# Kernel optimization log

Hardware: AMD Instinct MI355X
Metric: run time of the kernel (lower is better)

Reference implementation:

```python
import jax, jax.numpy as jnp
import numpy as np
import math

D_MODEL = 1024
N_HEADS = 16
HEAD_DIM = D_MODEL // N_HEADS
TEMP = 0.1          # sinkhorn temperature
SINK_ITERS = 10     # update_permutation uses n_iterations=10
EPS = 1e-10


def setup_inputs() -> dict:
    key = jax.random.key(0)
    ks = jax.random.split(key, 16)
    b, n, d = 2, 2048, D_MODEL
    x_data = jax.random.normal(ks[0], (b, n, d), dtype=jnp.float32)
    certainty = jax.random.uniform(ks[1], (b, n), dtype=jnp.float32)
    permutation = jnp.stack([jax.random.permutation(jax.random.fold_in(ks[2], i), n)
                             for i in range(b)]).astype(jnp.int64)
    def lin(k):
        kw, kb = jax.random.split(k)
        W = jax.random.normal(kw, (d, d), dtype=jnp.float32) * 0.02
        bvec = jax.random.normal(kb, (d,), dtype=jnp.float32) * 0.02
        return W, bvec
    Wq, bq = lin(ks[3]); Wk, bk = lin(ks[4]); Wv, bv = lin(ks[5]); Wo, bo = lin(ks[6])
    perm_bias_scale = jnp.ones((1, N_HEADS, 1, 1), dtype=jnp.float32)
    certainty_temp = jnp.ones((1,), dtype=jnp.float32) * 2.0
    return {"x_data": x_data, "certainty": certainty, "permutation": permutation,
            "Wq": Wq, "bq": bq, "Wk": Wk, "bk": bk, "Wv": Wv, "bv": bv,
            "Wo": Wo, "bo": bo, "perm_bias_scale": perm_bias_scale,
            "certainty_temp": certainty_temp}


def reference(x_data, certainty, permutation, Wq, bq, Wk, bk, Wv, bv, Wo, bo,
              perm_bias_scale, certainty_temp):
    b, n, d = x_data.shape
    scale = math.sqrt(HEAD_DIM)

    def proj(W, bias):  # nn.Linear: x @ W.T + b, then split heads -> (b,H,n,hd)
        y = jnp.einsum('bnd,ed->bne', x_data, W) + bias
        return y.reshape(b, n, N_HEADS, HEAD_DIM).transpose(0, 2, 1, 3)

    Q, K, V = proj(Wq, bq), proj(Wk, bk), proj(Wv, bv)

    scores = jnp.einsum('bhnk,bhmk->bhnm', Q, K) / scale  # (b,H,n,n)
    # permutation-distance bias: B[i,j] = -|sigma(i)-sigma(j)| * |scale_h|
    pf = permutation.astype(jnp.float32)
    dist = jnp.abs(pf[:, :, None] - pf[:, None, :])       # (b,n,n)
    scores = scores - dist[:, None, :, :] * jnp.abs(perm_bias_scale)

    attention = jax.nn.softmax(scores, axis=-1)           # dropout is identity (eval)
    out = jnp.einsum('bhnm,bhmd->bhnd', attention, V)
    out = out.transpose(0, 2, 1, 3).reshape(b, n, d)
    output = jnp.einsum('bnd,ed->bne', out, Wo) + bo

    # certainty update from attention entropy
    ent = -(attention * jnp.log(attention + EPS)).sum(-1).mean(1)  # (b,n)
    cert_upd = jax.nn.sigmoid(certainty_temp * (math.log(n) - ent))
    new_certainty = jnp.maximum(certainty, cert_upd)

    # permutation update via Sinkhorn on log mean attention
    avg_attn = attention.mean(axis=1)
    P = jnp.exp(jnp.log(avg_attn + EPS) / TEMP)
    def body(_, P):
        P = P / (P.sum(-1, keepdims=True) + EPS)
        P = P / (P.sum(-2, keepdims=True) + EPS)
        return P
    P = jax.lax.fori_loop(0, SINK_ITERS, body, P)
    idx = jnp.argmax(P, axis=-1)                          # (b,n)
    new_permutation = jnp.take_along_axis(permutation, idx, axis=1)

    return output, new_certainty, new_permutation
```

## Files before the change

### kernel.cpp

```cpp
#include <hip/hip_runtime.h>
#include <cstdint>

#define NTOK 2048
#define DMODEL 1024
#define NHEADS 16
#define HD 64
#define BATCH 2
#define EPSF 1e-10f
#define EPSD 1e-10

typedef __attribute__((ext_vector_type(8))) short bf16x8;
typedef __attribute__((ext_vector_type(8))) _Float16 f16x8;
typedef __attribute__((ext_vector_type(4))) float f32x4;

__device__ __forceinline__ float bf2f(unsigned short u){
  union { unsigned int i; float f; } c; c.i = ((unsigned int)u) << 16; return c.f;
}
__device__ __forceinline__ unsigned short f2bf(float f){
  union { float f; unsigned int u; } c; c.f = f;
  unsigned int u = c.u;
  unsigned int r = (u + 0x7FFFu + ((u >> 16) & 1u)) >> 16;
  return (unsigned short)r;
}
__device__ __forceinline__ unsigned short f2h(float f){
  union { _Float16 h; unsigned short u; } c; c.h = (_Float16)f; return c.u;
}
__device__ __forceinline__ float h2f(unsigned short u){
  union { unsigned short u; _Float16 h; } c; c.u = u; return (float)c.h;
}

__device__ __forceinline__ void async16(const unsigned short* g, unsigned short* lds_base){
  __builtin_amdgcn_global_load_lds((const __attribute__((address_space(1))) unsigned int*)g,
                                   (__attribute__((address_space(3))) unsigned int*)lds_base,
                                   16, 0, 0);
}

template<int BM, int BN>
__device__ __forceinline__ void gemm_bt_core(
    const unsigned short* A, int lda,
    const unsigned short* B, int ldb,
    int K,
    f32x4 (&acc)[BM/32][BN/32],
    unsigned short* ldsA, unsigned short* ldsB)
{
  constexpr int TM = BM/32, TN = BN/32;
  const int tid  = threadIdx.x;
  const int lane = tid & 63;
  const int wave = tid >> 6;
  const int wm = wave >> 1, wn = wave & 1;
  const int fr = lane & 15;
  const int fk = (lane >> 4) << 3;
  const int sr = lane >> 2;
  const int sk = (lane & 3) << 3;

  for (int k0 = 0; k0 < K; k0 += 32){
    #pragma unroll
    for (int c = 0; c < BM/64; c++){
      int ch = c*4 + wave;
      async16(A + (long)(ch*16 + sr)*lda + (k0 + sk), ldsA + ch*512);
    }
    #pragma unroll
    for (int c = 0; c < BN/64; c++){
      int ch = c*4 + wave;
      async16(B + (long)(ch*16 + sr)*ldb + (k0 + sk), ldsB + ch*512);
    }
    __syncthreads();
    bf16x8 af[TM], bf[TN];
    #pragma unroll
    for (int i=0;i<TM;i++)
      af[i] = *(const bf16x8*)(ldsA + ((wm*TM*16) + i*16 + fr)*32 + fk);
    #pragma unroll
    for (int j=0;j<TN;j++)
      bf[j] = *(const bf16x8*)(ldsB + ((wn*TN*16) + j*16 + fr)*32 + fk);
    #pragma unroll
    for (int i=0;i<TM;i++)
      #pragma unroll
      for (int j=0;j<TN;j++)
        acc[i][j] = __builtin_amdgcn_mfma_f32_16x16x32_bf16(af[i], bf[j], acc[i][j], 0, 0, 0);
    __syncthreads();
  }
}

__device__ __forceinline__ double wred_sumd(double x){
  for(int o=32;o;o>>=1) x+=__shfl_xor(x,o); return x;
}


__global__ void f2b_multi(const float* __restrict__ x,
    const float* __restrict__ wq, const float* __restrict__ wk,
    const float* __restrict__ wv, const float* __restrict__ wo,
    unsigned short* __restrict__ out)
{
  int i = blockIdx.x*256 + threadIdx.x;
  int base = i << 2;
  const float* src;
  if (base < 4194304) src = x + base;
  else {
    int d = base - 4194304;
    int r = d >> 20, off = d & 1048575;
    src = (r==0 ? wq : (r==1 ? wk : (r==2 ? wv : wo))) + off;
  }
  float4 v = *(const float4*)src;
  ushort4 o;
  o.x = f2bf(v.x); o.y = f2bf(v.y); o.z = f2bf(v.z); o.w = f2bf(v.w);
  *(ushort4*)(out + base) = o;
}

__global__ void init_kernel(double* __restrict__ uv){
  int idx = blockIdx.x*256 + threadIdx.x;
  if (idx < 8192) uv[idx] = 1.0;
}

__global__ __launch_bounds__(256) void qkv_kernel(
    const unsigned short* __restrict__ xb,
    const unsigned short* __restrict__ Wqb, const float* __restrict__ bq,
    const unsigned short* __restrict__ Wkb, const float* __restrict__ bk,
    const unsigned short* __restrict__ Wvb, const float* __restrict__ bv,
    unsigned short* __restrict__ Qb, unsigned short* __restrict__ Kb,
    unsigned short* __restrict__ Vb)
{
  __shared__ unsigned short lds[(128+128)*32];
  int sel = blockIdx.y >> 3;
  int n0 = (blockIdx.y & 7) * 128;
  int m0 = blockIdx.x * 128;
  const unsigned short* W = sel==0 ? Wqb : (sel==1 ? Wkb : Wvb);
  const float* bias       = sel==0 ? bq  : (sel==1 ? bk  : bv);
  unsigned short* out     = sel==0 ? Qb  : (sel==1 ? Kb  : Vb);
  f32x4 acc[4][4];
  f32x4 z = {0.f,0.f,0.f,0.f};
  for (int i=0;i<4;i++) for(int j=0;j<4;j++) acc[i][j] = z;
  gemm_bt_core<128,128>(xb + (long)m0*DMODEL, DMODEL, W + (long)n0*DMODEL, DMODEL,
                        DMODEL, acc, lds, lds + 128*32);
  int lane = threadIdx.x & 63, wave = threadIdx.x >> 6;
  int wm = wave>>1, wn = wave&1;
  int cr = (lane>>4)<<2, cc = lane & 15;
  for (int i=0;i<4;i++) for(int j=0;j<4;j++) for(int r=0;r<4;r++){
    int row = m0 + wm*64 + i*16 + cr + r;
    int col = n0 + wn*64 + j*16 + cc;
    out[(long)row*DMODEL + col] = f2bf(acc[i][j][r] + bias[col]);
  }
}

__global__ void vtrans_kernel(const unsigned short* __restrict__ Vb,
                              unsigned short* __restrict__ Vt)
{
  __shared__ unsigned short t[32][33];
  int b = blockIdx.z, i0 = blockIdx.x*32, e0 = blockIdx.y*32;
  int tx = threadIdx.x, ty = threadIdx.y;
  for (int r=0;r<32;r+=8) t[ty+r][tx] = Vb[((long)b*NTOK + i0+ty+r)*DMODEL + e0+tx];
  __syncthreads();
  for (int r=0;r<32;r+=8)
    Vt[((long)b*DMODEL + e0+ty+r)*NTOK + i0+tx] = f2h(bf2f(t[tx][ty+r]));
}

__global__ __launch_bounds__(512,4) void attnA_kernel(
    const unsigned short* __restrict__ Qb, const unsigned short* __restrict__ Kb,
    const unsigned short* __restrict__ Vt, const int* __restrict__ perm,
    const float* __restrict__ psc,
    float* __restrict__ mpart, float* __restrict__ lpart, float* __restrict__ Tpart,
    unsigned short* __restrict__ Opart)
{
  __shared__ unsigned short Kt[2*128*32];
  __shared__ unsigned short Vtl[64*136];
  __shared__ unsigned short Pt[128*136];
  __shared__ unsigned short pbs[2048];

  const int tid  = threadIdx.x;
  const int lane = tid & 63;
  const int wave = tid >> 6;
  const int fr   = lane & 15;
  const int fkg  = lane >> 4;
  const int fk   = fkg << 3;
  const int cr   = fkg << 2;
  const int rw   = wave << 4;
  const int rt   = blockIdx.x >> 1;
  const int half = blockIdx.x & 1;
  const int m0   = rt * 128;
  const int h    = blockIdx.y;
  const int b    = blockIdx.z;

  for (int i = tid; i < 2048; i += 512) pbs[i] = (unsigned short)perm[b*NTOK + i];

  bf16x8 qf[2];
  #pragma unroll
  for (int kc=0;kc<2;kc++)
    qf[kc] = *(const bf16x8*)(Qb + ((long)(b*NTOK + m0 + rw + fr))*DMODEL + h*HD + kc*32 + fk);

  const float asc = fabsf(psc[h]);
  __syncthreads();

  float prow[4];
  #pragma unroll
  for (int r=0;r<4;r++) prow[r] = (float)pbs[m0 + rw + cr + r];

  float mrow[4], lrow[4], Trow[4];
  #pragma unroll
  for (int r=0;r<4;r++){ mrow[r] = -1e30f; lrow[r] = 0.f; Trow[r] = 0.f; }
  f32x4 oacc[4];
  {
    f32x4 z = {0.f,0.f,0.f,0.f};
    for (int jj=0;jj<4;jj++) oacc[jj]=z;
  }

  for (int j2=0;j2<8;j2++){
    int j = half*8 + j2;
    __syncthreads();
    #pragma unroll
    for (int c=0;c<2;c++){
      int q = c*8 + wave;
      int kc = q >> 3, rb = (q & 7) * 16;
      async16(Kb + ((long)(b*NTOK + j*128 + rb + (lane>>2)))*DMODEL + h*HD + kc*32 + ((lane&3)<<3),
              Kt + kc*4096 + rb*32);
    }
    {
      int c = tid>>3, sg = tid&7;
      const unsigned short* vg = Vt + ((long)(b*DMODEL + h*HD + c))*NTOK + j*128 + sg*16;
      unsigned short* vl = Vtl + c*136 + sg*16;
      *(uint4*)(vl)   = *(const uint4*)(vg);
      *(uint4*)(vl+8) = *(const uint4*)(vg+8);
    }
    __syncthreads();

    f32x4 sacc[8];
    {
      f32x4 z = {0.f,0.f,0.f,0.f};
      for (int jj=0;jj<8;jj++) sacc[jj]=z;
    }
    #pragma unroll
    for (int kc=0;kc<2;kc++){
      bf16x8 bfr[8];
      #pragma unroll
      for (int jj=0;jj<8;jj++) bfr[jj] = *(const bf16x8*)(Kt + kc*4096 + (jj*16+fr)*32 + fk);
      #pragma unroll
      for (int jj=0;jj<8;jj++)
        sacc[jj] = __builtin_amdgcn_mfma_f32_16x16x32_bf16(qf[kc], bfr[jj], sacc[jj],0,0,0);
    }

    float pcol[8];
    #pragma unroll
    for (int jj=0;jj<8;jj++) pcol[jj] = (float)pbs[j*128 + jj*16 + fr];

    #pragma unroll
    for (int r=0;r<4;r++){
      float sv[8];
      float tm = -1e30f;
      #pragma unroll
      for (int jj=0;jj<8;jj++){
        sv[jj] = sacc[jj][r]*0.125f - fabsf(prow[r]-pcol[jj])*asc;
        tm = fmaxf(tm, sv[jj]);
      }
      #pragma unroll
      for (int o=1;o<16;o<<=1) tm = fmaxf(tm, __shfl_xor(tm,o));
      float nm = fmaxf(mrow[r], tm);
      float alpha = __expf(mrow[r] - nm);
      float lres = lrow[r]*alpha;
      Trow[r] = Trow[r]*alpha + (mrow[r]-nm)*lres;
      #pragma unroll
      for (int jc=0;jc<4;jc++) oacc[jc][r] *= alpha;
      float ts=0.f, tT=0.f;
      int prowbase = (rw + cr + r)*136;
      #pragma unroll
      for (int jj=0;jj<8;jj++){
        float d = sv[jj]-nm;
        float ev = __expf(d);
        ts += ev; tT += ev*d;
        Pt[prowbase + jj*16 + fr] = f2h(ev);
      }
      #pragma unroll
      for (int o=1;o<16;o<<=1){ ts += __shfl_xor(ts,o); tT += __shfl_xor(tT,o); }
      lrow[r] = lres + ts;
      Trow[r] += tT;
      mrow[r] = nm;
    }
    __syncthreads();
    #pragma unroll
    for (int kp=0;kp<4;kp++){
      f16x8 paf, pbf[4];
      paf = *(const f16x8*)(Pt + (rw+fr)*136 + kp*32 + fk);
      #pragma unroll
      for (int jj=0;jj<4;jj++) pbf[jj] = *(const f16x8*)(Vtl + (jj*16+fr)*136 + kp*32 + fk);
      #pragma unroll
      for (int jj=0;jj<4;jj++)
        oacc[jj] = __builtin_amdgcn_mfma_f32_16x16x32_f16(paf, pbf[jj], oacc[jj],0,0,0);
    }
  }

  long pbase = ((long)(half*BATCH + b)*NHEADS + h)*NTOK;
  #pragma unroll
  for (int jj=0;jj<4;jj++)
    #pragma unroll
    for (int r=0;r<4;r++){
      int row = m0 + rw + cr + r;
      Opart[(pbase + row)*HD + jj*16 + fr] = f2bf(oacc[jj][r]);
    }
  if (fr == 0){
    #pragma unroll
    for (int r=0;r<4;r++){
      int row = m0 + rw + cr + r;
      mpart[pbase + row] = mrow[r];
      lpart[pbase + row] = lrow[r];
      Tpart[pbase + row] = Trow[r];
    }
  }
}

__global__ __launch_bounds__(256) void merge_kernel(
    const float* __restrict__ mpart, const float* __restrict__ lpart,
    const float* __restrict__ Tpart, const unsigned short* __restrict__ Opart,
    unsigned short* __restrict__ Ob, float* __restrict__ mbuf,
    float* __restrict__ ilbuf, float* __restrict__ entb)
{
  int tid = threadIdx.x;
  int row = blockIdx.x*4 + (tid>>6);
  int h = blockIdx.y;
  int b = blockIdx.z;
  int col = tid & 63;
  long o1 = ((long)(0*BATCH + b)*NHEADS + h)*NTOK + row;
  long o2 = ((long)(1*BATCH + b)*NHEADS + h)*NTOK + row;
  float m1 = mpart[o1], m2 = mpart[o2];
  float l1 = lpart[o1], l2 = lpart[o2];
  float m = fmaxf(m1, m2);
  float e1 = __expf(m1-m), e2 = __expf(m2-m);
  float l = l1*e1 + l2*e2;
  float il = 1.0f/l;
  float Ov = (bf2f(Opart[o1*HD + col])*e1 + bf2f(Opart[o2*HD + col])*e2)*il;
  Ob[((long)(b*NTOK + row))*DMODEL + h*HD + col] = f2bf(Ov);
  if (col == 0){
    float T = e1*(Tpart[o1] + (m1-m)*l1) + e2*(Tpart[o2] + (m2-m)*l2);
    long off = ((long)(b*NHEADS+h))*NTOK + row;
    mbuf[off] = m; ilbuf[off] = il;
    entb[off] = T*il - __logf(l);
  }
}

__global__ __launch_bounds__(512,4) void avgP_kernel(
    const unsigned short* __restrict__ Qb, const unsigned short* __restrict__ Kb,
    const int* __restrict__ perm, const float* __restrict__ psc,
    const float* __restrict__ mbuf, const float* __restrict__ ilbuf,
    float* __restrict__ avg, unsigned short* __restrict__ avgH,
    unsigned short* __restrict__ avgT)
{
  __shared__ unsigned short Kt[2][8192];
  __shared__ float sm[NHEADS*64];
  __shared__ float si[NHEADS*64];
  __shared__ float sasc[NHEADS];

  const int bid = blockIdx.x;
  const int xcd = bid & 7, idx = bid >> 3;
  const int b   = xcd >> 2;
  const int qy  = (xcd >> 1) & 1, qx = xcd & 1;
  const int ydim = qy*16 + (idx >> 3);
  const int xdim = qx*8  + (idx & 7);
  const int m0   = ydim * 64;
  const int colb = xdim * 128;

  const int tid  = threadIdx.x;
  const int lane = tid & 63;
  const int wave = tid >> 6;
  const int wr = wave >> 2, wc = wave & 3;
  const int rw = wr*32, cb = wc*32;
  const int fr = lane & 15;
  const int fk = (lane >> 4) << 3;
  const int cr = (lane >> 4) << 2;
  const int cc = lane & 15;
  const int sr = lane >> 2;
  const int sk = (lane & 3) << 3;

  const unsigned short* kgp[2];
  int ldsoff[2];
  #pragma unroll
  for (int q=0;q<2;q++){
    int cid = q*8 + wave;
    int kc = cid >> 3, ch = cid & 7;
    kgp[q] = Kb + ((long)(b*NTOK + colb + ch*16 + sr))*DMODEL + kc*32 + sk;
    ldsoff[q] = kc*4096 + ch*512;
  }

  for (int e = tid; e < NHEADS*64; e += 512){
    int h = e >> 6, r = e & 63;
    long off = ((long)(b*NHEADS + h))*NTOK + m0 + r;
    sm[e] = mbuf[off];
    si[e] = ilbuf[off];
  }
  if (tid < NHEADS) sasc[tid] = fabsf(psc[tid]);

  float prw[8];
  #pragma unroll
  for (int i=0;i<2;i++)
    #pragma unroll
    for (int r=0;r<4;r++)
      prw[i*4+r] = (float)perm[b*NTOK + m0 + rw + i*16 + cr + r];
  float pcl[2];
  #pragma unroll
  for (int j=0;j<2;j++)
    pcl[j] = (float)perm[b*NTOK + colb + cb + j*16 + cc];

  const unsigned short* qp[2];
  #pragma unroll
  for (int i=0;i<2;i++)
    qp[i] = Qb + ((long)(b*NTOK + m0 + rw + i*16 + fr))*DMODEL + fk;

  float aacc[2][2][4];
  #pragma unroll
  for (int i=0;i<2;i++) for (int j=0;j<2;j++) for (int r=0;r<4;r++) aacc[i][j][r]=0.f;

  #pragma unroll
  for (int q=0;q<2;q++) async16(kgp[q], &Kt[0][0] + ldsoff[q]);
  __syncthreads();

  unsigned short* curb = &Kt[0][0];
  unsigned short* nxtb = &Kt[1][0];

  #pragma unroll 2
  for (int h=0; h<NHEADS; h++){
    if (h < NHEADS-1){
      #pragma unroll
      for (int q=0;q<2;q++) async16(kgp[q] + (h+1)*HD, nxtb + ldsoff[q]);
    }
    bf16x8 qf[2][2];
    #pragma unroll
    for (int i=0;i<2;i++)
      #pragma unroll
      for (int kc=0;kc<2;kc++)
        qf[i][kc] = *(const bf16x8*)(qp[i] + h*HD + kc*32);

    f32x4 acc[2][2];
    {
      f32x4 z = {0.f,0.f,0.f,0.f};
      acc[0][0]=z; acc[0][1]=z; acc[1][0]=z; acc[1][1]=z;
    }
    #pragma unroll
    for (int kc=0;kc<2;kc++){
      bf16x8 bfr[2];
      #pragma unroll
      for (int j=0;j<2;j++)
        bfr[j] = *(const bf16x8*)(curb + kc*4096 + ((cb>>4) + j)*512 + fr*32 + fk);
      #pragma unroll
      for (int i=0;i<2;i++)
        #pragma unroll
        for (int j=0;j<2;j++)
          acc[i][j] = __builtin_amdgcn_mfma_f32_16x16x32_bf16(qf[i][kc], bfr[j], acc[i][j],0,0,0);
    }
    const float asc = sasc[h];
    #pragma unroll
    for (int i=0;i<2;i++)
      #pragma unroll
      for (int r=0;r<4;r++){
        int rl = rw + i*16 + cr + r;
        float mh = sm[h*64 + rl];
        float ih = si[h*64 + rl];
        #pragma unroll
        for (int j=0;j<2;j++){
          float sv = acc[i][j][r]*0.125f - fabsf(prw[i*4+r]-pcl[j])*asc;
          aacc[i][j][r] += __expf(sv - mh) * ih;
        }
      }
    __syncthreads();
    unsigned short* t = curb; curb = nxtb; nxtb = t;
  }

  unsigned short* T = &Kt[0][0];
  #pragma unroll
  for (int i=0;i<2;i++)
    #pragma unroll
    for (int j=0;j<2;j++)
      #pragma unroll
      for (int r=0;r<4;r++){
        float pw = __expf(__logf(aacc[i][j][r]*0.0625f + EPSF)*10.0f);
        int rl = rw + i*16 + cr + r;
        int cl = cb + j*16 + cc;
        long off = ((long)(b*NTOK + m0 + rl))*NTOK + colb + cl;
        avg[off] = pw;
        unsigned short hv = f2h(pw);
        avgH[off] = hv;
        T[cl*72 + rl] = hv;
      }
  __syncthreads();
  {
    int c = tid >> 2, sg = tid & 3;
    uint4* dst = (uint4*)(avgT + ((long)(b*NTOK + colb + c))*NTOK + m0 + sg*16);
    const unsigned short* src = T + c*72 + sg*16;
    dst[0] = *(const uint4*)(src);
    dst[1] = *(const uint4*)(src + 8);
  }
}

__global__ __launch_bounds__(256) void sink_phase_h(const unsigned short* __restrict__ M,
    const double* __restrict__ x, double* __restrict__ y)
{
  int b = blockIdx.y, tid = threadIdx.x;
  int wave = tid >> 6, lane = tid & 63;
  int i = blockIdx.x*4 + wave;
  const unsigned short* row = M + ((long)b*NTOK + i)*NTOK;
  const double* xb = x + b*NTOK;
  double s = 0.0;
  #pragma unroll
  for (int k=0;k<4;k++){
    int j = k*512 + lane*8;
    f16x8 mv = *(const f16x8*)(row + j);
    #pragma unroll
    for (int e=0;e<8;e++) s += (double)(float)mv[e] * xb[j+e];
  }
  s = wred_sumd(s);
  if (lane == 0){
    double yi = y[b*NTOK + i];
    y[b*NTOK + i] = yi / (yi*s + EPSD);
  }
}

__global__ __launch_bounds__(256) void argmax_kernel(const float* __restrict__ P,
    const double* __restrict__ v, const int* __restrict__ perm,
    float* __restrict__ dout_perm)
{
  int b = blockIdx.y, tid = threadIdx.x;
  int wave = tid >> 6, lane = tid & 63;
  int i = blockIdx.x*4 + wave;
  const float* row = P + ((long)b*NTOK + i)*NTOK;
  const double* vb = v + b*NTOK;
  double bv = -1.0; int bj = 0;
  #pragma unroll
  for (int k=0;k<4;k++){
    int j0 = k*512 + lane*8;
    float4 r0 = *(const float4*)(row + j0);
    float4 r1 = *(const float4*)(row + j0 + 4);
    float rv[8] = {r0.x,r0.y,r0.z,r0.w,r1.x,r1.y,r1.z,r1.w};
    #pragma unroll
    for (int e=0;e<8;e++){
      double val = (double)rv[e]*vb[j0+e];
      if (val>bv){ bv=val; bj=j0+e; }
    }
  }
  for (int o=32;o;o>>=1){
    double ov=__shfl_xor(bv,o); int oj=__shfl_xor(bj,o);
    if (ov>bv || (ov==bv && oj<bj)){bv=ov;bj=oj;}
  }
  if (lane == 0)
    dout_perm[b*NTOK + i] = (float)perm[b*NTOK + bj];
}

__global__ __launch_bounds__(256) void out_kernel(
    const unsigned short* __restrict__ Ob, const unsigned short* __restrict__ Wob,
    const float* __restrict__ bo, float* __restrict__ dout)
{
  __shared__ unsigned short lds[(128+128)*32];
  int m0 = blockIdx.x*128, n0 = blockIdx.y*128;
  f32x4 acc[4][4];
  f32x4 z = {0.f,0.f,0.f,0.f};
  for (int i=0;i<4;i++) for(int j=0;j<4;j++) acc[i][j] = z;
  gemm_bt_core<128,128>(Ob + (long)m0*DMODEL, DMODEL, Wob + (long)n0*DMODEL, DMODEL,
                        DMODEL, acc, lds, lds + 128*32);
  int lane = threadIdx.x & 63, wave = threadIdx.x >> 6;
  int wm = wave>>1, wn = wave&1;
  int cr = (lane>>4)<<2, cc = lane & 15;
  for (int i=0;i<4;i++) for(int j=0;j<4;j++) for(int r=0;r<4;r++){
    int row = m0 + wm*64 + i*16 + cr + r;
    int col = n0 + wn*64 + j*16 + cc;
    dout[(long)row*DMODEL + col] = acc[i][j][r] + bo[col];
  }
}

__global__ void cert_kernel(const float* __restrict__ cert,
    const float* __restrict__ ctemp, const float* __restrict__ entb,
    float* __restrict__ dout_cert)
{
  int idx = blockIdx.x*256+threadIdx.x;
  if (idx >= BATCH*NTOK) return;
  int b = idx >> 11, row = idx & 2047;
  float s = 0.f;
  #pragma unroll
  for (int h=0; h<NHEADS; h++) s += entb[((long)(b*NHEADS+h))*NTOK + row];
  float ent = -s * (1.0f/16.0f);
  float ct = ctemp[0];
  float arg = ct * (logf((float)NTOK) - ent);
  float upd = 1.0f/(1.0f+expf(-arg));
  dout_cert[idx] = fmaxf(cert[idx], upd);
}

extern "C" void kernel_launch(void* const* d_in, const int* in_sizes, int n_in,
                              void* d_out, int out_size, void* d_ws, size_t ws_size,
                              hipStream_t stream)
{
  const float* x    = (const float*)d_in[0];
  const float* cert = (const float*)d_in[1];
  const int*   perm = (const int*)d_in[2];
  const float* Wq   = (const float*)d_in[3];
  const float* bq   = (const float*)d_in[4];
  const float* Wk   = (const float*)d_in[5];
  const float* bk   = (const float*)d_in[6];
  const float* Wv   = (const float*)d_in[7];
  const float* bv   = (const float*)d_in[8];
  const float* Wo   = (const float*)d_in[9];
  const float* bo   = (const float*)d_in[10];
  const float* psc  = (const float*)d_in[11];
  const float* ctmp = (const float*)d_in[12];
  float* dout = (float*)d_out;

  double* u    = (double*)d_ws;
  double* v    = u + 4096;
  float* avg   = (float*)(v + 4096);
  float* mbuf  = avg   + 8388608;
  float* ilbuf = mbuf  + 65536;
  float* entb  = ilbuf + 65536;
  float* mpart = entb  + 65536;
  float* lpart = mpart + 131072;
  float* Tpart = lpart + 131072;
  unsigned short* Opart = (unsigned short*)(Tpart + 131072);
  unsigned short* xb  = Opart + 8388608;
  unsigned short* Wqb = xb  + 4194304;
  unsigned short* Wkb = Wqb + 1048576;
  unsigned short* Wvb = Wkb + 1048576;
  unsigned short* Wob = Wvb + 1048576;
  unsigned short* Qb  = Wob + 1048576;
  unsigned short* Kb  = Qb  + 4194304;
  unsigned short* Vb  = Kb  + 4194304;
  unsigned short* Vt  = Vb  + 4194304;
  unsigned short* Ob  = Vt  + 4194304;
  unsigned short* avgH = Opart;
  unsigned short* avgT = Vb;

  f2b_multi<<<dim3(8192),256,0,stream>>>(x, Wq, Wk, Wv, Wo, xb);
  init_kernel<<<dim3(32),256,0,stream>>>(u);

  qkv_kernel<<<dim3(32,24),256,0,stream>>>(xb, Wqb,bq, Wkb,bk, Wvb,bv, Qb,Kb,Vb);
  vtrans_kernel<<<dim3(64,32,2), dim3(32,8),0,stream>>>(Vb, Vt);

  attnA_kernel<<<dim3(32,NHEADS,2),512,0,stream>>>(Qb, Kb, Vt, perm, psc,
      mpart, lpart, Tpart, Opart);
  merge_kernel<<<dim3(512,NHEADS,2),256,0,stream>>>(mpart, lpart, Tpart, Opart,
      Ob, mbuf, ilbuf, entb);
  avgP_kernel<<<dim3(1024),512,0,stream>>>(Qb, Kb, perm, psc, mbuf, ilbuf,
      avg, avgH, avgT);

  for (int it=0; it<10; it++){
    sink_phase_h<<<dim3(512,2),256,0,stream>>>(avgH, v, u);
    sink_phase_h<<<dim3(512,2),256,0,stream>>>(avgT, u, v);
  }
  argmax_kernel<<<dim3(512,2),256,0,stream>>>(avg, v, perm, dout + 4194304 + 4096);

  out_kernel <<<dim3(32,8),256,0,stream>>>(Ob, Wob, bo, dout);
  cert_kernel<<<dim3(16), 256,0,stream>>>(cert, ctmp, entb, dout + 4194304);
}
```

Measured before the change: 498.4 us.

## Shrink attention KV tile to 64 and add lazy softmax max rescaling

The attention kernel now processes 64 keys per iteration instead of 128, with 16 iterations per half. This cuts shared memory and per-thread accumulators, and the launch bound is raised to allow more resident blocks. It also switches to lazy online-softmax rescaling: the running max and the O/l/T accumulators are only updated when a tile's max exceeds the stored max by more than 8. This avoids most exp/multiply rescales at the cost of fp16 probabilities up to about e^8. The new 68-element LDS row stride is not a multiple of 16 bytes, so 128-bit LDS loads on odd rows become misaligned, and the twice-as-many iterations double the number of barriers.

```diff
diff --git a/kernel.cpp b/kernel.cpp
--- a/kernel.cpp
+++ b/kernel.cpp
@@ -153,16 +153,16 @@
     Vt[((long)b*DMODEL + e0+ty+r)*NTOK + i0+tx] = f2h(bf2f(t[tx][ty+r]));
 }
 
-__global__ __launch_bounds__(512,4) void attnA_kernel(
+__global__ __launch_bounds__(512,8) void attnA_kernel(
     const unsigned short* __restrict__ Qb, const unsigned short* __restrict__ Kb,
     const unsigned short* __restrict__ Vt, const int* __restrict__ perm,
     const float* __restrict__ psc,
     float* __restrict__ mpart, float* __restrict__ lpart, float* __restrict__ Tpart,
     unsigned short* __restrict__ Opart)
 {
-  __shared__ unsigned short Kt[2*128*32];
-  __shared__ unsigned short Vtl[64*136];
-  __shared__ unsigned short Pt[128*136];
+  __shared__ unsigned short Kt[2*64*32];
+  __shared__ unsigned short Vtl[64*68];
+  __shared__ unsigned short Pt[128*68];
   __shared__ unsigned short pbs[2048];
 
   const int tid  = threadIdx.x;
@@ -202,83 +202,81 @@
     for (int jj=0;jj<4;jj++) oacc[jj]=z;
   }
 
-  for (int j2=0;j2<8;j2++){
-    int j = half*8 + j2;
+  for (int j2=0;j2<16;j2++){
+    int j = half*16 + j2;
     __syncthreads();
-    #pragma unroll
-    for (int c=0;c<2;c++){
-      int q = c*8 + wave;
-      int kc = q >> 3, rb = (q & 7) * 16;
-      async16(Kb + ((long)(b*NTOK + j*128 + rb + (lane>>2)))*DMODEL + h*HD + kc*32 + ((lane&3)<<3),
-              Kt + kc*4096 + rb*32);
+    {
+      int kc = wave >> 2, ch = wave & 3;
+      async16(Kb + ((long)(b*NTOK + j*64 + ch*16 + (lane>>2)))*DMODEL + h*HD + kc*32 + ((lane&3)<<3),
+              Kt + kc*2048 + ch*512);
     }
     {
       int c = tid>>3, sg = tid&7;
-      const unsigned short* vg = Vt + ((long)(b*DMODEL + h*HD + c))*NTOK + j*128 + sg*16;
-      unsigned short* vl = Vtl + c*136 + sg*16;
-      *(uint4*)(vl)   = *(const uint4*)(vg);
-      *(uint4*)(vl+8) = *(const uint4*)(vg+8);
+      const unsigned short* vg = Vt + ((long)(b*DMODEL + h*HD + c))*NTOK + j*64 + sg*8;
+      *(uint4*)(Vtl + c*68 + sg*8) = *(const uint4*)(vg);
     }
     __syncthreads();
 
-    f32x4 sacc[8];
+    f32x4 sacc[4];
     {
       f32x4 z = {0.f,0.f,0.f,0.f};
-      for (int jj=0;jj<8;jj++) sacc[jj]=z;
+      for (int jj=0;jj<4;jj++) sacc[jj]=z;
     }
     #pragma unroll
     for (int kc=0;kc<2;kc++){
-      bf16x8 bfr[8];
-      #pragma unroll
-      for (int jj=0;jj<8;jj++) bfr[jj] = *(const bf16x8*)(Kt + kc*4096 + (jj*16+fr)*32 + fk);
-      #pragma unroll
-      for (int jj=0;jj<8;jj++)
+      bf16x8 bfr[4];
+      #pragma unroll
+      for (int jj=0;jj<4;jj++) bfr[jj] = *(const bf16x8*)(Kt + kc*2048 + (jj*16+fr)*32 + fk);
+      #pragma unroll
+      for (int jj=0;jj<4;jj++)
         sacc[jj] = __builtin_amdgcn_mfma_f32_16x16x32_bf16(qf[kc], bfr[jj], sacc[jj],0,0,0);
     }
 
-    float pcol[8];
-    #pragma unroll
-    for (int jj=0;jj<8;jj++) pcol[jj] = (float)pbs[j*128 + jj*16 + fr];
+    float pcol[4];
+    #pragma unroll
+    for (int jj=0;jj<4;jj++) pcol[jj] = (float)pbs[j*64 + jj*16 + fr];
 
     #pragma unroll
     for (int r=0;r<4;r++){
-      float sv[8];
+      float sv[4];
       float tm = -1e30f;
       #pragma unroll
-      for (int jj=0;jj<8;jj++){
+      for (int jj=0;jj<4;jj++){
         sv[jj] = sacc[jj][r]*0.125f - fabsf(prow[r]-pcol[jj])*asc;
         tm = fmaxf(tm, sv[jj]);
       }
       #pragma unroll
       for (int o=1;o<16;o<<=1) tm = fmaxf(tm, __shfl_xor(tm,o));
-      float nm = fmaxf(mrow[r], tm);
-      float alpha = __expf(mrow[r] - nm);
-      float lres = lrow[r]*alpha;
-      Trow[r] = Trow[r]*alpha + (mrow[r]-nm)*lres;
-      #pragma unroll
-      for (int jc=0;jc<4;jc++) oacc[jc][r] *= alpha;
+      float d0 = tm - mrow[r];
+      if (d0 > 8.0f){
+        float al = __expf(-d0);
+        #pragma unroll
+        for (int jc=0;jc<4;jc++) oacc[jc][r] *= al;
+        Trow[r] = Trow[r]*al - d0*(lrow[r]*al);
+        lrow[r] *= al;
+        mrow[r] = tm;
+      }
       float ts=0.f, tT=0.f;
-      int prowbase = (rw + cr + r)*136;
-      #pragma unroll
-      for (int jj=0;jj<8;jj++){
-        float d = sv[jj]-nm;
+      int prowbase = (rw + cr + r)*68;
+      #pragma unroll
+      for (int jj=0;jj<4;jj++){
+        float d = sv[jj]-mrow[r];
         float ev = __expf(d);
         ts += ev; tT += ev*d;
         Pt[prowbase + jj*16 + fr] = f2h(ev);
       }
       #pragma unroll
       for (int o=1;o<16;o<<=1){ ts += __shfl_xor(ts,o); tT += __shfl_xor(tT,o); }
-      lrow[r] = lres + ts;
+      lrow[r] += ts;
       Trow[r] += tT;
-      mrow[r] = nm;
     }
     __syncthreads();
     #pragma unroll
-    for (int kp=0;kp<4;kp++){
+    for (int kp=0;kp<2;kp++){
       f16x8 paf, pbf[4];
-      paf = *(const f16x8*)(Pt + (rw+fr)*136 + kp*32 + fk);
-      #pragma unroll
-      for (int jj=0;jj<4;jj++) pbf[jj] = *(const f16x8*)(Vtl + (jj*16+fr)*136 + kp*32 + fk);
+      paf = *(const f16x8*)(Pt + (rw+fr)*68 + kp*32 + fk);
+      #pragma unroll
+      for (int jj=0;jj<4;jj++) pbf[jj] = *(const f16x8*)(Vtl + (jj*16+fr)*68 + kp*32 + fk);
       #pragma unroll
       for (int jj=0;jj<4;jj++)
         oacc[jj] = __builtin_amdgcn_mfma_f32_16x16x32_f16(paf, pbf[jj], oacc[jj],0,0,0);
```

Measured after the change: 1.005 ms. 102% more time.
